# Performance work log

Measured on AMD Instinct MI355X. Metric: run time of the kernel, lower is better.

## Reference

```python
import jax, jax.numpy as jnp
import numpy as np

N = 50000      # nodes
E = 1_000_000  # edges
EMB = 64       # out_channels per head
H = 2          # heads
HC = H * EMB   # 128 = concat output dim
HID = 128      # fc hidden size
NEG_SLOPE = 0.2


def _p(k, shape):
    return jax.random.normal(k, shape, dtype=jnp.float32) * 0.1


def setup_inputs() -> dict:
    key = jax.random.key(0)
    ks = jax.random.split(key, 24)
    inp = {
        "x": jax.random.normal(ks[0], (N, 1), dtype=jnp.float32),
        "edge_index": jax.random.randint(ks[1], (2, E), 0, N, dtype=jnp.int32),
        "edge_attr": jax.random.normal(ks[2], (E, 1), dtype=jnp.float32),
        "target_node_idx": 123,
        # conv1: GATv2Conv(1 -> 64, heads=2, edge_dim=1)
        "Wl1": _p(ks[3], (1, HC)), "bl1": jnp.zeros((HC,), jnp.float32),
        "Wr1": _p(ks[4], (1, HC)), "br1": jnp.zeros((HC,), jnp.float32),
        "We1": _p(ks[5], (1, HC)),
        "att1": _p(ks[6], (H, EMB)),
        "b1": jnp.zeros((HC,), jnp.float32),
        # conv2: GATv2Conv(128 -> 64, heads=2, edge_dim=1)
        "Wl2": _p(ks[7], (HC, HC)), "bl2": jnp.zeros((HC,), jnp.float32),
        "Wr2": _p(ks[8], (HC, HC)), "br2": jnp.zeros((HC,), jnp.float32),
        "We2": _p(ks[9], (1, HC)),
        "att2": _p(ks[10], (H, EMB)),
        "b2": jnp.zeros((HC,), jnp.float32),
        # fc: Linear(128 -> 128)
        "Wfc": _p(ks[11], (HC, HID)), "bfc": jnp.zeros((HID,), jnp.float32),
    }
    return inp


def add_self_loops(src, dst, edge_attr, n):
    loop = jnp.arange(n, dtype=src.dtype)
    fill = jnp.mean(edge_attr, axis=0)  # PyG fill_value='mean'
    src2 = jnp.concatenate([src, loop])
    dst2 = jnp.concatenate([dst, loop])
    ea2 = jnp.concatenate([edge_attr, jnp.broadcast_to(fill, (n, edge_attr.shape[1]))])
    return src2, dst2, ea2


def gatv2(x, src, dst, edge_attr, Wl, bl, Wr, br, We, att, bias, n):
    # x: [n, F_in]; per-head transforms -> [n, H, EMB]
    xl = (x @ Wl + bl).reshape(n, H, EMB)   # source transform
    xr = (x @ Wr + br).reshape(n, H, EMB)   # target transform
    ef = (edge_attr @ We).reshape(-1, H, EMB)
    # GATv2 attention: a^T LeakyReLU(xl_j + xr_i + e_ij)
    z = jax.nn.leaky_relu(xl[src] + xr[dst] + ef, NEG_SLOPE)  # [E', H, EMB]
    logits = jnp.einsum('ehc,hc->eh', z, att)                 # [E', H]
    # segment softmax over incoming edges per destination node
    m = jax.ops.segment_max(logits, dst, num_segments=n)[dst]
    ex = jnp.exp(logits - m)
    s = jax.ops.segment_sum(ex, dst, num_segments=n)[dst]
    alpha = ex / s                                            # [E', H]
    msg = xl[src] * alpha[:, :, None]                         # [E', H, EMB]
    out = jax.ops.segment_sum(msg, dst, num_segments=n)       # [n, H, EMB]
    return out.reshape(n, HC) + bias


def reference(x, edge_index, edge_attr, target_node_idx,
              Wl1, bl1, Wr1, br1, We1, att1, b1,
              Wl2, bl2, Wr2, br2, We2, att2, b2,
              Wfc, bfc):
    n = x.shape[0]
    src, dst, ea = add_self_loops(edge_index[0], edge_index[1], edge_attr, n)
    h = gatv2(x, src, dst, ea, Wl1, bl1, Wr1, br1, We1, att1, b1, n)
    h = jax.nn.relu(h)
    h = gatv2(h, src, dst, ea, Wl2, bl2, Wr2, br2, We2, att2, b2, n)
    target_emb = h[target_node_idx]          # [HC]
    return target_emb @ Wfc + bfc            # [HID]
```

## Files before the change

kernel.cpp:

```cpp
#include <hip/hip_runtime.h>
#include <hip/hip_bf16.h>

#define NEG_SLOPE 0.2f
#define THR    256
#define NB1    512
#define NB2    512
#define B1CAP  16
#define B2CAP  32
#define CAP1   512
#define CAPS   64
#define MAXDEG 256
#define NTAIL  (CAPS + 1)

#define OFF_PARTS  8
#define OFF_B1CNT  (OFF_PARTS + NB1)
#define OFF_B1SRC  (OFF_B1CNT + NB1)
#define OFF_B1EA   (OFF_B1SRC + NB1 * B1CAP)
#define OFF_B2CNT  (OFF_B1EA + NB1 * B1CAP)
#define OFF_B2SRC  (OFF_B2CNT + NB2)
#define OFF_B2DST  (OFF_B2SRC + NB2 * B2CAP)
#define OFF_B2EA   (OFF_B2DST + NB2 * B2CAP)
#define OFF_L1SRC  (OFF_B2EA + NB2 * B2CAP)
#define OFF_L1EA   (OFF_L1SRC + CAP1)
#define OFF_SLIST  (OFF_L1EA + CAP1)
#define OFF_XL2    (OFF_SLIST + CAPS)
#define OFF_XR2    (OFF_XL2 + CAPS * 128)

__device__ __forceinline__ float us2f(unsigned short s) {
    union { unsigned int u; float f; } c;
    c.u = ((unsigned int)s) << 16;
    return c.f;
}
template<bool F32>
__device__ __forceinline__ float tld(const void* p, int i) {
    if (F32) return ((const float*)p)[i];
    return us2f(((const unsigned short*)p)[i]);
}
__device__ __forceinline__ float ald_f(const float* p) {
    return __hip_atomic_load(p, __ATOMIC_RELAXED, __HIP_MEMORY_SCOPE_AGENT);
}

template<bool F32>
__device__ void scan1_body(const int* __restrict__ src, const int* __restrict__ dst,
                           const void* __restrict__ ea, int t, int E,
                           int* __restrict__ W) {
    __shared__ float sRed[4];
    __shared__ int   sCnt;
    __shared__ int   sIb[B1CAP];
    __shared__ float sFb[B1CAP];
    const int tid = threadIdx.x, bid = blockIdx.x;
    const int gid = bid * THR + tid, gs = NB1 * THR;
    const int E4 = E >> 2, rem = E & 3;
    float* parts = (float*)(W + OFF_PARTS);
    int*   b1cnt = W + OFF_B1CNT;
    int*   b1src = W + OFF_B1SRC;
    float* b1ea  = (float*)(W + OFF_B1EA);

    if (tid == 0) sCnt = 0;
    __syncthreads();
    float sum = 0.f;
    for (int j = gid; j < E4; j += gs) {
        int4 d4 = ((const int4*)dst)[j];
        float v0, v1, v2, v3;
        if (F32) {
            float4 e4 = ((const float4*)ea)[j];
            v0 = e4.x; v1 = e4.y; v2 = e4.z; v3 = e4.w;
        } else {
            ushort4 u4 = ((const ushort4*)ea)[j];
            v0 = us2f(u4.x); v1 = us2f(u4.y); v2 = us2f(u4.z); v3 = us2f(u4.w);
        }
        sum += (v0 + v1) + (v2 + v3);
        int base = 4 * j;
        if (d4.x == t) { int p = atomicAdd(&sCnt, 1); if (p < B1CAP) { sIb[p] = src[base+0]; sFb[p] = v0; } }
        if (d4.y == t) { int p = atomicAdd(&sCnt, 1); if (p < B1CAP) { sIb[p] = src[base+1]; sFb[p] = v1; } }
        if (d4.z == t) { int p = atomicAdd(&sCnt, 1); if (p < B1CAP) { sIb[p] = src[base+2]; sFb[p] = v2; } }
        if (d4.w == t) { int p = atomicAdd(&sCnt, 1); if (p < B1CAP) { sIb[p] = src[base+3]; sFb[p] = v3; } }
    }
    if (gid < rem) {
        int i = E4 * 4 + gid;
        float v = tld<F32>(ea, i);
        sum += v;
        if (dst[i] == t) { int p = atomicAdd(&sCnt, 1); if (p < B1CAP) { sIb[p] = src[i]; sFb[p] = v; } }
    }
    for (int o = 32; o > 0; o >>= 1) sum += __shfl_down(sum, o);
    if ((tid & 63) == 0) sRed[tid >> 6] = sum;
    __syncthreads();
    if (tid == 0) parts[bid] = sRed[0] + sRed[1] + sRed[2] + sRed[3];
    int bc = sCnt < B1CAP ? sCnt : B1CAP;
    if (tid == 0) b1cnt[bid] = bc;
    if (tid < bc) { b1src[bid * B1CAP + tid] = sIb[tid]; b1ea[bid * B1CAP + tid] = sFb[tid]; }
}

__global__ void __launch_bounds__(THR)
k_scan1(const void* __restrict__ x, const int* __restrict__ src,
        const int* __restrict__ dst, const void* __restrict__ ea,
        const int* __restrict__ tgt, int E, int* __restrict__ W) {
    __shared__ int sWeird;
    if (threadIdx.x == 0) sWeird = 0;
    __syncthreads();
    {
        const unsigned short* u = (const unsigned short*)x;
        int c = 0;
        for (int i = threadIdx.x; i < 2048; i += THR) {
            int e2 = (u[i] >> 7) & 0xFF;
            if (e2 == 0 || e2 >= 0xC0) c++;
        }
        for (int o = 32; o > 0; o >>= 1) c += __shfl_down(c, o);
        if ((threadIdx.x & 63) == 0) atomicAdd(&sWeird, c);
    }
    __syncthreads();
    bool f32 = sWeird >= 64;
    if (blockIdx.x == 0 && threadIdx.x == 0) W[3] = f32 ? 1 : 0;
    int t = tgt[0];
    if (f32) scan1_body<true >(src, dst, ea, t, E, W);
    else     scan1_body<false>(src, dst, ea, t, E, W);
}

template<bool F32>
__device__ void scan2_body(const int* __restrict__ src, const int* __restrict__ dst,
                           const void* __restrict__ ea, int tgt0, int E,
                           int* __restrict__ W) {
    __shared__ int   sS[CAPS];
    __shared__ int   sNs, sCnt;
    __shared__ int   sIb[B2CAP], sIb2[B2CAP];
    __shared__ float sFb[B2CAP];
    __shared__ int   sPfx[THR];
    __shared__ float sRed[4];
    const int tid = threadIdx.x, bid = blockIdx.x;
    const int gid = bid * THR + tid, gs = NB2 * THR;
    const int E4 = E >> 2, rem = E & 3;
    float* parts = (float*)(W + OFF_PARTS);
    int*   b1cnt = W + OFF_B1CNT;
    int*   b1src = W + OFF_B1SRC;
    float* b1ea  = (float*)(W + OFF_B1EA);
    int*   b2cnt = W + OFF_B2CNT;
    int*   b2src = W + OFF_B2SRC;
    int*   b2dst = W + OFF_B2DST;
    float* b2ea  = (float*)(W + OFF_B2EA);
    int*   l1src = W + OFF_L1SRC;
    float* l1ea  = (float*)(W + OFF_L1EA);
    int*   slist = W + OFF_SLIST;

    if (tid == 0) { sS[0] = tgt0; sNs = 1; sCnt = 0; }
    __syncthreads();
    for (int bk = tid; bk < NB1; bk += THR) {
        int c = b1cnt[bk]; if (c > B1CAP) c = B1CAP;
        for (int j = 0; j < c; j++) {
            int p = atomicAdd(&sNs, 1);
            if (p < CAPS) sS[p] = b1src[bk * B1CAP + j];
        }
    }
    __syncthreads();
    int ns = sNs < CAPS ? sNs : CAPS;

    #define CHECK(dv, idx)                                                     \
        do {                                                                   \
            for (int j_ = 0; j_ < ns; j_++) {                                  \
                if (sS[j_] == (dv)) {                                          \
                    int p_ = atomicAdd(&sCnt, 1);                              \
                    if (p_ < B2CAP) {                                          \
                        sIb[p_] = src[idx]; sIb2[p_] = (dv);                   \
                        sFb[p_] = tld<F32>(ea, idx);                           \
                    }                                                          \
                    break;                                                     \
                }                                                              \
            }                                                                  \
        } while (0)
    for (int j = gid; j < E4; j += gs) {
        int4 d4 = ((const int4*)dst)[j];
        int base = 4 * j;
        CHECK(d4.x, base + 0);
        CHECK(d4.y, base + 1);
        CHECK(d4.z, base + 2);
        CHECK(d4.w, base + 3);
    }
    if (gid < rem) { int i = E4 * 4 + gid; CHECK(dst[i], i); }
    #undef CHECK
    __syncthreads();
    int bc = sCnt < B2CAP ? sCnt : B2CAP;
    if (tid == 0) b2cnt[bid] = bc;
    if (tid < bc) {
        b2src[bid * B2CAP + tid] = sIb[tid];
        b2dst[bid * B2CAP + tid] = sIb2[tid];
        b2ea [bid * B2CAP + tid] = sFb[tid];
    }

    if (bid == 0) {
        __syncthreads();
        int c0  = b1cnt[2*tid];    if (c0  > B1CAP) c0  = B1CAP;
        int c1b = b1cnt[2*tid+1];  if (c1b > B1CAP) c1b = B1CAP;
        int c = c0 + c1b;
        sPfx[tid] = c;
        __syncthreads();
        for (int o = 1; o < THR; o <<= 1) {
            int v = (tid >= o) ? sPfx[tid - o] : 0;
            __syncthreads();
            sPfx[tid] += v;
            __syncthreads();
        }
        int base = sPfx[tid] - c;
        int c1tot = sPfx[THR - 1];
        for (int j = 0; j < c0; j++) {
            int p = base + j;
            if (p < CAP1 - 1) { l1src[p] = b1src[2*tid*B1CAP + j]; l1ea[p] = b1ea[2*tid*B1CAP + j]; }
        }
        for (int j = 0; j < c1b; j++) {
            int p = base + c0 + j;
            if (p < CAP1 - 1) { l1src[p] = b1src[(2*tid+1)*B1CAP + j]; l1ea[p] = b1ea[(2*tid+1)*B1CAP + j]; }
        }
        float s = parts[tid] + parts[tid + THR];
        for (int o = 32; o > 0; o >>= 1) s += __shfl_down(s, o);
        if ((tid & 63) == 0) sRed[tid >> 6] = s;
        __syncthreads();
        if (tid == 0) {
            float mean = (sRed[0] + sRed[1] + sRed[2] + sRed[3]) / (float)E;
            int c1 = c1tot < CAP1 - 1 ? c1tot : CAP1 - 1;
            l1src[c1] = tgt0; l1ea[c1] = mean;
            c1++;
            int nsl = 0;
            for (int e = 0; e < c1; e++) {
                int sv = l1src[e];
                bool f = false;
                for (int j = 0; j < nsl; j++) if (sS[j] == sv) { f = true; break; }
                if (!f && nsl < CAPS) { sS[nsl] = sv; nsl++; }
            }
            for (int j = 0; j < nsl; j++) slist[j] = sS[j];
            W[0] = c1; W[1] = nsl; W[4] = 0;
            ((float*)W)[5] = mean;
        }
    }
}

__global__ void __launch_bounds__(THR)
k_scan2(const int* __restrict__ src, const int* __restrict__ dst,
        const void* __restrict__ ea, const int* __restrict__ tgt,
        int E, int* __restrict__ W) {
    int t = tgt[0];
    if (W[3]) scan2_body<true >(src, dst, ea, t, E, W);
    else      scan2_body<false>(src, dst, ea, t, E, W);
}

template<bool F32>
__device__ void tail_body(
    const void* __restrict__ x, int tgt0,
    const void* Wl1, const void* bl1, const void* Wr1, const void* br1,
    const void* We1, const void* att1, const void* b1,
    const void* Wl2, const void* bl2, const void* Wr2, const void* br2,
    const void* We2, const void* att2, const void* b2v,
    const void* Wfc, const void* bfc,
    void* __restrict__ out, int* __restrict__ W)
{
    const int tid = threadIdx.x, bid = blockIdx.x;
    int*   b2cnt = W + OFF_B2CNT;
    int*   b2src = W + OFF_B2SRC;
    int*   b2dst = W + OFF_B2DST;
    float* b2ea  = (float*)(W + OFF_B2EA);
    int*   l1src = W + OFF_L1SRC;
    float* l1ea  = (float*)(W + OFF_L1EA);
    int*   slist = W + OFF_SLIST;
    float* xl2   = (float*)(W + OFF_XL2);
    float* xr2   = (float*)(W + OFF_XR2);

    int ns = W[1]; if (ns > CAPS) ns = CAPS;
    int c1 = W[0]; if (c1 > CAP1) c1 = CAP1;
    float mean = ((float*)W)[5];

    if (bid < ns) {
        __shared__ float sWl[128], sBl[128], sWe[128], sAtt[128], sB1[128], sBase[128];
        __shared__ float sXs[MAXDEG], sEa2[MAXDEG], sL0[MAXDEG], sL1[MAXDEG], sH[128];
        __shared__ int sCnt;
        int s = slist[bid];
        if (tid < 128) {
            sWl[tid] = tld<F32>(Wl1, tid);  sBl[tid] = tld<F32>(bl1, tid);
            sWe[tid] = tld<F32>(We1, tid);  sAtt[tid] = tld<F32>(att1, tid);
            sB1[tid] = tld<F32>(b1, tid);
            float xt = tld<F32>(x, s);
            sBase[tid] = xt * tld<F32>(Wr1, tid) + tld<F32>(br1, tid);
        }
        if (tid == 0) { sCnt = 1; sXs[0] = tld<F32>(x, s); sEa2[0] = mean; }
        __syncthreads();
        for (int bk = tid; bk < NB2; bk += THR) {
            int c = b2cnt[bk]; if (c > B2CAP) c = B2CAP;
            for (int j = 0; j < c; j++) {
                if (b2dst[bk * B2CAP + j] == s) {
                    int p = atomicAdd(&sCnt, 1);
                    if (p < MAXDEG) {
                        sXs[p] = tld<F32>(x, b2src[bk * B2CAP + j]);
                        sEa2[p] = b2ea[bk * B2CAP + j];
                    }
                }
            }
        }
        __syncthreads();
        int deg = sCnt < MAXDEG ? sCnt : MAXDEG;
        for (int i = tid; i < deg; i += THR) {
            float xs = sXs[i], eav = sEa2[i];
            float l0 = 0.f, l1v = 0.f;
            #pragma unroll 8
            for (int c2 = 0; c2 < 128; c2++) {
                float v = xs * sWl[c2] + sBl[c2] + sBase[c2] + eav * sWe[c2];
                v = v > 0.f ? v : NEG_SLOPE * v;
                float w = v * sAtt[c2];
                if (c2 < 64) l0 += w; else l1v += w;
            }
            sL0[i] = l0; sL1[i] = l1v;
        }
        __syncthreads();
        if (tid == 0) {
            float m0 = -1e30f, m1 = -1e30f;
            for (int i = 0; i < deg; i++) { m0 = fmaxf(m0, sL0[i]); m1 = fmaxf(m1, sL1[i]); }
            float s0 = 0.f, s1 = 0.f;
            for (int i = 0; i < deg; i++) {
                sL0[i] = __expf(sL0[i] - m0); s0 += sL0[i];
                sL1[i] = __expf(sL1[i] - m1); s1 += sL1[i];
            }
            float r0 = 1.f / s0, r1 = 1.f / s1;
            for (int i = 0; i < deg; i++) { sL0[i] *= r0; sL1[i] *= r1; }
        }
        __syncthreads();
        if (tid < 128) {
            bool hi = tid >= 64;
            float acc = 0.f;
            for (int i = 0; i < deg; i++) {
                float a = hi ? sL1[i] : sL0[i];
                acc += a * (sXs[i] * sWl[tid] + sBl[tid]);
            }
            acc += sB1[tid];
            sH[tid] = fmaxf(acc, 0.f);
        }
        __syncthreads();
        if (tid < 128) {
            float acc = tld<F32>(bl2, tid);
            #pragma unroll 16
            for (int k = 0; k < 128; k++) acc += sH[k] * tld<F32>(Wl2, k * 128 + tid);
            xl2[bid * 128 + tid] = acc;
            if (s == tgt0) {
                float a2 = tld<F32>(br2, tid);
                #pragma unroll 16
                for (int k = 0; k < 128; k++) a2 += sH[k] * tld<F32>(Wr2, k * 128 + tid);
                xr2[tid] = a2;
            }
        }
        __syncthreads();
        __threadfence();
        if (tid == 0)
            __hip_atomic_fetch_add(&W[4], 1, __ATOMIC_RELEASE, __HIP_MEMORY_SCOPE_AGENT);
    } else if (bid == CAPS) {
        __shared__ float sl0[CAP1], sl1[CAP1];
        __shared__ int sslot[CAP1];
        __shared__ float semb[128];
        __shared__ int sS[CAPS];
        if (tid == 0) {
            while (__hip_atomic_load(&W[4], __ATOMIC_RELAXED, __HIP_MEMORY_SCOPE_AGENT) < ns)
                __builtin_amdgcn_s_sleep(32);
        }
        __syncthreads();
        __threadfence();
        if (tid < ns) sS[tid] = slist[tid];
        __syncthreads();
        for (int e = tid; e < c1; e += THR) {
            int sv = l1src[e];
            int slot = 0;
            for (int j = 0; j < ns; j++) if (sS[j] == sv) { slot = j; break; }
            sslot[e] = slot;
        }
        __syncthreads();
        float xr = 0.f, we = 0.f, at = 0.f;
        if (tid < 128) { xr = ald_f(&xr2[tid]); we = tld<F32>(We2, tid); at = tld<F32>(att2, tid); }
        for (int e = 0; e < c1; e++) {
            float w = 0.f;
            if (tid < 128) {
                float v = ald_f(&xl2[sslot[e] * 128 + tid]) + xr + l1ea[e] * we;
                v = v > 0.f ? v : NEG_SLOPE * v;
                w = v * at;
            }
            for (int o = 32; o > 0; o >>= 1) w += __shfl_down(w, o);
            if (tid == 0)  sl0[e] = w;
            if (tid == 64) sl1[e] = w;
        }
        __syncthreads();
        if (tid == 0) {
            float m0 = -1e30f, m1 = -1e30f;
            for (int e = 0; e < c1; e++) { m0 = fmaxf(m0, sl0[e]); m1 = fmaxf(m1, sl1[e]); }
            float s0 = 0.f, s1 = 0.f;
            for (int e = 0; e < c1; e++) {
                sl0[e] = __expf(sl0[e] - m0); s0 += sl0[e];
                sl1[e] = __expf(sl1[e] - m1); s1 += sl1[e];
            }
            float r0 = 1.f / s0, r1 = 1.f / s1;
            for (int e = 0; e < c1; e++) { sl0[e] *= r0; sl1[e] *= r1; }
        }
        __syncthreads();
        if (tid < 128) {
            bool hi = tid >= 64;
            float acc = tld<F32>(b2v, tid);
            for (int e = 0; e < c1; e++) {
                float a = hi ? sl1[e] : sl0[e];
                acc += a * ald_f(&xl2[sslot[e] * 128 + tid]);
            }
            semb[tid] = acc;
        }
        __syncthreads();
        if (tid < 128) {
            float o = tld<F32>(bfc, tid);
            #pragma unroll 16
            for (int c2 = 0; c2 < 128; c2++) o += semb[c2] * tld<F32>(Wfc, c2 * 128 + tid);
            if (F32) ((float*)out)[tid] = o;
            else     ((__hip_bfloat16*)out)[tid] = __float2bfloat16(o);
        }
    }
}

__global__ void __launch_bounds__(THR)
k_tail(const void* x, const int* tgt,
       const void* Wl1, const void* bl1, const void* Wr1, const void* br1,
       const void* We1, const void* att1, const void* b1,
       const void* Wl2, const void* bl2, const void* Wr2, const void* br2,
       const void* We2, const void* att2, const void* b2v,
       const void* Wfc, const void* bfc,
       void* out, int* W)
{
    int t = tgt[0];
    if (W[3]) tail_body<true >(x, t, Wl1, bl1, Wr1, br1, We1, att1, b1,
                               Wl2, bl2, Wr2, br2, We2, att2, b2v, Wfc, bfc, out, W);
    else      tail_body<false>(x, t, Wl1, bl1, Wr1, br1, We1, att1, b1,
                               Wl2, bl2, Wr2, br2, We2, att2, b2v, Wfc, bfc, out, W);
}

extern "C" void kernel_launch(void* const* d_in, const int* in_sizes, int n_in,
                              void* d_out, int out_size, void* d_ws, size_t ws_size,
                              hipStream_t stream) {
    const void* x    = d_in[0];
    const int*  eidx = (const int*)d_in[1];
    const void* eattr= d_in[2];
    const int*  tgt  = (const int*)d_in[3];
    const void* Wl1 = d_in[4],  *bl1 = d_in[5],  *Wr1 = d_in[6],  *br1 = d_in[7];
    const void* We1 = d_in[8],  *att1= d_in[9],  *b1  = d_in[10];
    const void* Wl2 = d_in[11], *bl2 = d_in[12], *Wr2 = d_in[13], *br2 = d_in[14];
    const void* We2 = d_in[15], *att2= d_in[16], *b2v = d_in[17];
    const void* Wfc = d_in[18], *bfc = d_in[19];

    int E = in_sizes[1] / 2;
    const int* src = eidx;
    const int* dst = eidx + E;
    int* W = (int*)d_ws;

    k_scan1<<<NB1, THR, 0, stream>>>(x, src, dst, eattr, tgt, E, W);
    k_scan2<<<NB2, THR, 0, stream>>>(src, dst, eattr, tgt, E, W);
    k_tail <<<NTAIL, THR, 0, stream>>>(x, tgt, Wl1, bl1, Wr1, br1, We1, att1, b1,
                                       Wl2, bl2, Wr2, br2, We2, att2, b2v,
                                       Wfc, bfc, d_out, W);
}
```

Measured before the change: 157.9 us.

## Parallelize tail-kernel logits, softmax and matvecs across all threads and prefetch weights

The tail kernel's per-source and final blocks are restructured. Logits are now computed with two threads per edge, softmax reductions are done with wave shuffles instead of a single thread, and the 128x128 matvecs are split across all 256 threads with shared partial sums. The final block stages xl2 into padded shared memory, computes edge logits per thread instead of with a serial per-edge wave reduction, and touches Wfc before spinning on the completion counter to warm the cache. The intent is to shorten the serial critical path of this latency-bound tail, at the cost of more shared memory and extra barriers.

Result: faster. 147.1 us (-6.8%).

```diff
diff --git a/kernel.cpp b/kernel.cpp
--- a/kernel.cpp
+++ b/kernel.cpp
@@ -268,6 +268,7 @@
     if (bid < ns) {
         __shared__ float sWl[128], sBl[128], sWe[128], sAtt[128], sB1[128], sBase[128];
         __shared__ float sXs[MAXDEG], sEa2[MAXDEG], sL0[MAXDEG], sL1[MAXDEG], sH[128];
+        __shared__ float sPartL[THR];
         __shared__ int sCnt;
         int s = slist[bid];
         if (tid < 128) {
@@ -293,29 +294,35 @@
         }
         __syncthreads();
         int deg = sCnt < MAXDEG ? sCnt : MAXDEG;
-        for (int i = tid; i < deg; i += THR) {
-            float xs = sXs[i], eav = sEa2[i];
-            float l0 = 0.f, l1v = 0.f;
-            #pragma unroll 8
-            for (int c2 = 0; c2 < 128; c2++) {
-                float v = xs * sWl[c2] + sBl[c2] + sBase[c2] + eav * sWe[c2];
-                v = v > 0.f ? v : NEG_SLOPE * v;
-                float w = v * sAtt[c2];
-                if (c2 < 64) l0 += w; else l1v += w;
-            }
-            sL0[i] = l0; sL1[i] = l1v;
-        }
-        __syncthreads();
-        if (tid == 0) {
-            float m0 = -1e30f, m1 = -1e30f;
-            for (int i = 0; i < deg; i++) { m0 = fmaxf(m0, sL0[i]); m1 = fmaxf(m1, sL1[i]); }
-            float s0 = 0.f, s1 = 0.f;
-            for (int i = 0; i < deg; i++) {
-                sL0[i] = __expf(sL0[i] - m0); s0 += sL0[i];
-                sL1[i] = __expf(sL1[i] - m1); s1 += sL1[i];
-            }
-            float r0 = 1.f / s0, r1 = 1.f / s1;
-            for (int i = 0; i < deg; i++) { sL0[i] *= r0; sL1[i] *= r1; }
+        {
+            int i0 = tid >> 1, half = tid & 1, c0 = half << 6;
+            for (int i = i0; i < deg; i += 128) {
+                float xs = sXs[i], eav = sEa2[i];
+                float acc = 0.f;
+                #pragma unroll 8
+                for (int c2 = 0; c2 < 64; c2++) {
+                    int c = c0 + c2;
+                    float v = xs * sWl[c] + sBl[c] + sBase[c] + eav * sWe[c];
+                    v = v > 0.f ? v : NEG_SLOPE * v;
+                    acc += v * sAtt[c];
+                }
+                if (half == 0) sL0[i] = acc; else sL1[i] = acc;
+            }
+        }
+        __syncthreads();
+        {
+            int lane = tid & 63, wv = tid >> 6;
+            if (wv < 2) {
+                float* sl = wv ? sL1 : sL0;
+                float m = -1e30f;
+                for (int i = lane; i < deg; i += 64) m = fmaxf(m, sl[i]);
+                for (int o = 32; o > 0; o >>= 1) m = fmaxf(m, __shfl_xor(m, o));
+                float ss = 0.f;
+                for (int i = lane; i < deg; i += 64) { float t = __expf(sl[i] - m); sl[i] = t; ss += t; }
+                for (int o = 32; o > 0; o >>= 1) ss += __shfl_xor(ss, o);
+                float r = 1.f / ss;
+                for (int i = lane; i < deg; i += 64) sl[i] *= r;
+            }
         }
         __syncthreads();
         if (tid < 128) {
@@ -329,82 +336,121 @@
             sH[tid] = fmaxf(acc, 0.f);
         }
         __syncthreads();
-        if (tid < 128) {
-            float acc = tld<F32>(bl2, tid);
+        {
+            int outc = tid & 127, k0 = (tid >> 7) << 6;
+            float acc = 0.f;
             #pragma unroll 16
-            for (int k = 0; k < 128; k++) acc += sH[k] * tld<F32>(Wl2, k * 128 + tid);
-            xl2[bid * 128 + tid] = acc;
-            if (s == tgt0) {
-                float a2 = tld<F32>(br2, tid);
-                #pragma unroll 16
-                for (int k = 0; k < 128; k++) a2 += sH[k] * tld<F32>(Wr2, k * 128 + tid);
-                xr2[tid] = a2;
-            }
+            for (int k = 0; k < 64; k++) acc += sH[k0 + k] * tld<F32>(Wl2, (k0 + k) * 128 + outc);
+            sPartL[tid] = acc;
+        }
+        __syncthreads();
+        if (tid < 128) xl2[bid * 128 + tid] = tld<F32>(bl2, tid) + sPartL[tid] + sPartL[tid + 128];
+        if (s == tgt0) {
+            __syncthreads();
+            int outc = tid & 127, k0 = (tid >> 7) << 6;
+            float acc = 0.f;
+            #pragma unroll 16
+            for (int k = 0; k < 64; k++) acc += sH[k0 + k] * tld<F32>(Wr2, (k0 + k) * 128 + outc);
+            sPartL[tid] = acc;
+            __syncthreads();
+            if (tid < 128) xr2[tid] = tld<F32>(br2, tid) + sPartL[tid] + sPartL[tid + 128];
         }
         __syncthreads();
         __threadfence();
         if (tid == 0)
             __hip_atomic_fetch_add(&W[4], 1, __ATOMIC_RELEASE, __HIP_MEMORY_SCOPE_AGENT);
     } else if (bid == CAPS) {
+        __shared__ float sXl2[CAPS * 129];
+        __shared__ float sXr[128];
         __shared__ float sl0[CAP1], sl1[CAP1];
-        __shared__ int sslot[CAP1];
+        __shared__ float sEaF[CAP1];
+        __shared__ int   sslot[CAP1];
         __shared__ float semb[128];
-        __shared__ int sS[CAPS];
-        if (tid == 0) {
-            while (__hip_atomic_load(&W[4], __ATOMIC_RELAXED, __HIP_MEMORY_SCOPE_AGENT) < ns)
-                __builtin_amdgcn_s_sleep(32);
-        }
-        __syncthreads();
-        __threadfence();
-        if (tid < ns) sS[tid] = slist[tid];
+        __shared__ int   sSf[CAPS];
+        __shared__ float sWe2s[128], sAtt2s[128];
+        __shared__ float sPartF[THR];
+
+        if (tid < ns) sSf[tid] = slist[tid];
+        float b2vv = 0.f, bfcv = 0.f;
+        if (tid < 128) {
+            sWe2s[tid]  = tld<F32>(We2, tid);
+            sAtt2s[tid] = tld<F32>(att2, tid);
+            b2vv = tld<F32>(b2v, tid);
+            bfcv = tld<F32>(bfc, tid);
+        }
         __syncthreads();
         for (int e = tid; e < c1; e += THR) {
             int sv = l1src[e];
             int slot = 0;
-            for (int j = 0; j < ns; j++) if (sS[j] == sv) { slot = j; break; }
+            for (int j = 0; j < ns; j++) if (sSf[j] == sv) { slot = j; break; }
             sslot[e] = slot;
-        }
-        __syncthreads();
-        float xr = 0.f, we = 0.f, at = 0.f;
-        if (tid < 128) { xr = ald_f(&xr2[tid]); we = tld<F32>(We2, tid); at = tld<F32>(att2, tid); }
-        for (int e = 0; e < c1; e++) {
-            float w = 0.f;
-            if (tid < 128) {
-                float v = ald_f(&xl2[sslot[e] * 128 + tid]) + xr + l1ea[e] * we;
+            sEaF[e] = l1ea[e];
+        }
+        {
+            float pf = 0.f;
+            #pragma unroll 8
+            for (int i = tid; i < 128 * 128; i += THR) pf += tld<F32>(Wfc, i);
+            asm volatile("" :: "v"(pf));
+        }
+        if (tid == 0) {
+            while (__hip_atomic_load(&W[4], __ATOMIC_RELAXED, __HIP_MEMORY_SCOPE_AGENT) < ns)
+                __builtin_amdgcn_s_sleep(8);
+        }
+        __syncthreads();
+        __threadfence();
+        for (int i = tid; i < ns * 128; i += THR)
+            sXl2[(i >> 7) * 129 + (i & 127)] = ald_f(&xl2[i]);
+        if (tid < 128) sXr[tid] = ald_f(&xr2[tid]);
+        __syncthreads();
+        for (int e = tid; e < c1; e += THR) {
+            const float* row = &sXl2[sslot[e] * 129];
+            float ev = sEaF[e];
+            float l0 = 0.f, l1v = 0.f;
+            #pragma unroll 8
+            for (int c = 0; c < 128; c++) {
+                float v = row[c] + sXr[c] + ev * sWe2s[c];
                 v = v > 0.f ? v : NEG_SLOPE * v;
-                w = v * at;
-            }
-            for (int o = 32; o > 0; o >>= 1) w += __shfl_down(w, o);
-            if (tid == 0)  sl0[e] = w;
-            if (tid == 64) sl1[e] = w;
-        }
-        __syncthreads();
-        if (tid == 0) {
-            float m0 = -1e30f, m1 = -1e30f;
-            for (int e = 0; e < c1; e++) { m0 = fmaxf(m0, sl0[e]); m1 = fmaxf(m1, sl1[e]); }
-            float s0 = 0.f, s1 = 0.f;
-            for (int e = 0; e < c1; e++) {
-                sl0[e] = __expf(sl0[e] - m0); s0 += sl0[e];
-                sl1[e] = __expf(sl1[e] - m1); s1 += sl1[e];
-            }
-            float r0 = 1.f / s0, r1 = 1.f / s1;
-            for (int e = 0; e < c1; e++) { sl0[e] *= r0; sl1[e] *= r1; }
+                float w = v * sAtt2s[c];
+                if (c < 64) l0 += w; else l1v += w;
+            }
+            sl0[e] = l0; sl1[e] = l1v;
+        }
+        __syncthreads();
+        {
+            int lane = tid & 63, wv = tid >> 6;
+            if (wv < 2) {
+                float* sl = wv ? sl1 : sl0;
+                float m = -1e30f;
+                for (int e = lane; e < c1; e += 64) m = fmaxf(m, sl[e]);
+                for (int o = 32; o > 0; o >>= 1) m = fmaxf(m, __shfl_xor(m, o));
+                float ss = 0.f;
+                for (int e = lane; e < c1; e += 64) { float t = __expf(sl[e] - m); sl[e] = t; ss += t; }
+                for (int o = 32; o > 0; o >>= 1) ss += __shfl_xor(ss, o);
+                float r = 1.f / ss;
+                for (int e = lane; e < c1; e += 64) sl[e] *= r;
+            }
         }
         __syncthreads();
         if (tid < 128) {
             bool hi = tid >= 64;
-            float acc = tld<F32>(b2v, tid);
+            float acc = b2vv;
             for (int e = 0; e < c1; e++) {
                 float a = hi ? sl1[e] : sl0[e];
-                acc += a * ald_f(&xl2[sslot[e] * 128 + tid]);
+                acc += a * sXl2[sslot[e] * 129 + tid];
             }
             semb[tid] = acc;
         }
         __syncthreads();
+        {
+            int outc = tid & 127, k0 = (tid >> 7) << 6;
+            float acc = 0.f;
+            #pragma unroll 16
+            for (int k = 0; k < 64; k++) acc += semb[k0 + k] * tld<F32>(Wfc, (k0 + k) * 128 + outc);
+            sPartF[tid] = acc;
+        }
+        __syncthreads();
         if (tid < 128) {
-            float o = tld<F32>(bfc, tid);
-            #pragma unroll 16
-            for (int c2 = 0; c2 < 128; c2++) o += semb[c2] * tld<F32>(Wfc, c2 * 128 + tid);
+            float o = bfcv + sPartF[tid] + sPartF[tid + 128];
             if (F32) ((float*)out)[tid] = o;
             else     ((__hip_bfloat16*)out)[tid] = __float2bfloat16(o);
         }
```
